# Kernel tuning notes

Measured on AMD Instinct MI355X. Metric: run time of the kernel, lower is better.

The kernel has to match this reference:

```python
import jax, jax.numpy as jnp
import numpy as np

N_HEADS = 16
EMBED_DIM = 1024
HEAD_DIM = EMBED_DIM // N_HEADS
B, S = 4, 2048


def setup_inputs() -> dict:
    key = jax.random.key(0)
    k1, k2, k3, k4 = jax.random.split(key, 4)
    scale = 1.0 / np.sqrt(EMBED_DIM)
    x = jax.random.normal(k1, (B, S, EMBED_DIM), dtype=jnp.float32)
    Wq = jax.random.normal(k2, (EMBED_DIM, EMBED_DIM), dtype=jnp.float32) * scale
    Wk = jax.random.normal(k3, (EMBED_DIM, EMBED_DIM), dtype=jnp.float32) * scale
    Wv = jax.random.normal(k4, (EMBED_DIM, EMBED_DIM), dtype=jnp.float32) * scale
    return {"x": x, "Wq": Wq, "Wk": Wk, "Wv": Wv}


def reference(x, Wq, Wk, Wv):
    b, s, d = x.shape
    # torch nn.Linear(bias=False): y = x @ W.T
    def proj(W):
        return (x @ W.T).reshape(b, s, N_HEADS, HEAD_DIM).transpose(0, 2, 1, 3)  # [b,h,s,hd]
    q, k, v = proj(Wq), proj(Wk), proj(Wv)
    # scores scaled by sqrt(embed_dim) as in the source (not head_dim)
    scores = jnp.einsum('bhqd,bhkd->bhqk', q, k) / jnp.sqrt(jnp.float32(d))
    attn = jax.nn.softmax(scores, axis=-1)
    out = jnp.einsum('bhqk,bhkd->bhqd', attn, v)  # [b,h,s,hd]
    return out.transpose(0, 2, 1, 3).reshape(b, s, d)
```

## Files before the change

### kernel.cpp

```cpp
#include <hip/hip_runtime.h>

#define S_LEN  2048
#define NHEAD  16
#define HDIM   64
#define DMODEL 1024
#define XN     (4 * 2048 * 1024)
#define WN     (1024 * 1024)

typedef float  floatx4 __attribute__((ext_vector_type(4)));
typedef __bf16 bf16x8  __attribute__((ext_vector_type(8)));
typedef __bf16 bf16x4  __attribute__((ext_vector_type(4)));
typedef unsigned int u32;

union B8 {
  bf16x8 v8;
  bf16x4 v4[2];
  __bf16 e[8];
  uint4  u;
};

typedef __attribute__((address_space(1))) u32 gu32;
typedef __attribute__((address_space(3))) u32 lu32;
__device__ __forceinline__ void gld16(const void* g, void* l) {
  __builtin_amdgcn_global_load_lds((const gu32*)g, (lu32*)l, 16, 0, 0);
}

__global__ __launch_bounds__(256) void cvt_kernel(
    const float* __restrict__ x,  const float* __restrict__ Wq,
    const float* __restrict__ Wk, const float* __restrict__ Wv,
    __bf16* __restrict__ xb, __bf16* __restrict__ Wb)
{
  const size_t base = ((size_t)blockIdx.x * 256 + threadIdx.x) * 8;
  const float* src;
  __bf16* dst;
  float scl = 1.0f;
  if (base < XN) {
    src = x + base;
    dst = xb + base;
  } else {
    const size_t j = base - XN;
    const int mat = (int)(j >> 20);
    const size_t o = j & (WN - 1);
    src = (mat == 0 ? Wq : mat == 1 ? Wk : Wv) + o;
    dst = Wb + ((size_t)mat << 20) + o;
    if (mat == 0) scl = 0.045084220027780106f;
  }
  float4 a = *(const float4*)src;
  float4 b = *(const float4*)(src + 4);
  B8 r;
  r.e[0] = (__bf16)(a.x * scl); r.e[1] = (__bf16)(a.y * scl);
  r.e[2] = (__bf16)(a.z * scl); r.e[3] = (__bf16)(a.w * scl);
  r.e[4] = (__bf16)(b.x * scl); r.e[5] = (__bf16)(b.y * scl);
  r.e[6] = (__bf16)(b.z * scl); r.e[7] = (__bf16)(b.w * scl);
  *(bf16x8*)dst = r.v8;
}

__global__ __launch_bounds__(256) void proj_kernel(
    const __bf16* __restrict__ xb, const __bf16* __restrict__ Wb,
    __bf16* __restrict__ Qo, __bf16* __restrict__ Ko, __bf16* __restrict__ Vt)
{
  __shared__ __attribute__((aligned(16))) union {
    struct { __bf16 As[128 * 32]; __bf16 Bs[128 * 32]; } st;
    __bf16 Es[4][64][72];
  } sh;

  const int tid  = threadIdx.x;
  const int lane = tid & 63;
  const int wv   = tid >> 6;
  const int l15  = lane & 15;
  const int quad = lane >> 4;

  const int row0 = blockIdx.y * 128;
  const int n0   = blockIdx.x * 128;
  const int wrow = (wv >> 1) * 64;
  const int wcol = (wv & 1) * 64;

  floatx4 acc[4][4];
  #pragma unroll
  for (int i = 0; i < 4; i++)
    #pragma unroll
    for (int j = 0; j < 4; j++) acc[i][j] = (floatx4)0.0f;

  const int swz = quad ^ ((l15 >> 1) & 3);

  for (int kk = 0; kk < DMODEL; kk += 32) {
    #pragma unroll
    for (int i = 0; i < 2; i++) {
      const int c    = tid + i * 256;
      const int r    = c >> 2;
      const int glog = (c & 3) ^ ((c >> 3) & 3);
      const size_t lofs = (size_t)(wv * 64 + i * 256) * 8;
      gld16(xb + (size_t)(row0 + r) * DMODEL + kk + glog * 8, sh.st.As + lofs);
      gld16(Wb + (size_t)(n0 + r) * DMODEL + kk + glog * 8, sh.st.Bs + lofs);
    }
    __syncthreads();

    B8 af[4], bg[4];
    #pragma unroll
    for (int mb = 0; mb < 4; mb++)
      af[mb].u = *(const uint4*)(sh.st.As + (size_t)(wrow + mb * 16 + l15) * 32 + swz * 8);
    #pragma unroll
    for (int nb = 0; nb < 4; nb++)
      bg[nb].u = *(const uint4*)(sh.st.Bs + (size_t)(wcol + nb * 16 + l15) * 32 + swz * 8);

    #pragma unroll
    for (int mb = 0; mb < 4; mb++)
      #pragma unroll
      for (int nb = 0; nb < 4; nb++)
        acc[mb][nb] = __builtin_amdgcn_mfma_f32_16x16x32_bf16(
            af[mb].v8, bg[nb].v8, acc[mb][nb], 0, 0, 0);
    __syncthreads();
  }

  const int mat   = n0 >> 10;
  const int bb    = (row0 + wrow) >> 11;
  const int sbase = (row0 + wrow) & 2047;
  const int hh    = ((n0 & 1023) + wcol) >> 6;
  __syncthreads();

  if (mat < 2) {
    #pragma unroll
    for (int mb = 0; mb < 4; mb++)
      #pragma unroll
      for (int rr = 0; rr < 4; rr++)
        #pragma unroll
        for (int nb = 0; nb < 4; nb++)
          sh.Es[wv][mb * 16 + quad * 4 + rr][nb * 16 + l15] =
              (__bf16)acc[mb][nb][rr];
    __bf16* Out = (mat == 0) ? Qo : Ko;
    const size_t obase = ((size_t)(bb * NHEAD + hh) * S_LEN + sbase) * HDIM;
    #pragma unroll
    for (int t = 0; t < 8; t++) {
      const int lin = t * 64 + lane;
      const int s = lin >> 3, g = lin & 7;
      *(uint4*)&Out[obase + (size_t)s * HDIM + g * 8] =
          *(const uint4*)&sh.Es[wv][s][g * 8];
    }
  } else {
    #pragma unroll
    for (int mb = 0; mb < 4; mb++)
      #pragma unroll
      for (int nb = 0; nb < 4; nb++) {
        bf16x4 pk = { (__bf16)acc[mb][nb][0], (__bf16)acc[mb][nb][1],
                      (__bf16)acc[mb][nb][2], (__bf16)acc[mb][nb][3] };
        const int col = 32 * (mb >> 1) + 16 * (quad >> 1) + 8 * (quad & 1) +
                        4 * (mb & 1);
        *(bf16x4*)&sh.Es[wv][nb * 16 + l15][col] = pk;
      }
    const size_t vbase = (size_t)(bb * NHEAD + hh) * HDIM * S_LEN;
    #pragma unroll
    for (int t = 0; t < 8; t++) {
      const int lin = t * 64 + lane;
      const int d = lin >> 3, g = lin & 7;
      *(uint4*)&Vt[vbase + (size_t)d * S_LEN + sbase + g * 8] =
          *(const uint4*)&sh.Es[wv][d][g * 8];
    }
  }
}

__global__ __launch_bounds__(256, 2) void attn_kernel(
    const __bf16* __restrict__ Q, const __bf16* __restrict__ K,
    const __bf16* __restrict__ Vt, float* __restrict__ out)
{
  __shared__ __attribute__((aligned(16))) __bf16 Ks[64 * 64];
  __shared__ __attribute__((aligned(16))) __bf16 Vs[64 * 64];

  const int tid  = threadIdx.x;
  const int lane = tid & 63;
  const int wv   = tid >> 6;
  const int l15  = lane & 15;
  const int quad = lane >> 4;

  const int bh = blockIdx.x;
  const int q0 = blockIdx.y * 256;
  const int b  = bh >> 4;
  const int h  = bh & 15;

  const __bf16* Qb = Q  + (size_t)bh * S_LEN * HDIM;
  const __bf16* Kb = K  + (size_t)bh * S_LEN * HDIM;
  const __bf16* Vb = Vt + (size_t)bh * HDIM * S_LEN;

  B8 aq[4][2];
  #pragma unroll
  for (int nb = 0; nb < 4; nb++)
    #pragma unroll
    for (int kc = 0; kc < 2; kc++)
      aq[nb][kc].u = *(const uint4*)
          &Qb[(size_t)(q0 + wv * 64 + nb * 16 + l15) * HDIM + kc * 32 + quad * 8];

  floatx4 o[4][4];
  float rs[4];
  #pragma unroll
  for (int mt = 0; mt < 4; mt++)
    #pragma unroll
    for (int nb = 0; nb < 4; nb++) o[mt][nb] = (floatx4)0.0f;
  #pragma unroll
  for (int nb = 0; nb < 4; nb++) rs[nb] = 0.0f;

  const int swz0 = quad ^ (l15 & 7);
  const int swz1 = (4 + quad) ^ (l15 & 7);

  for (int kv0 = 0; kv0 < S_LEN; kv0 += 64) {
    #pragma unroll
    for (int i = 0; i < 2; i++) {
      const int c    = tid + i * 256;
      const int r    = c >> 3;
      const int glog = (c & 7) ^ ((c >> 3) & 7);
      const size_t lofs = (size_t)(wv * 64 + i * 256) * 8;
      gld16(Kb + (size_t)(kv0 + r) * HDIM + glog * 8, Ks + lofs);
      gld16(Vb + (size_t)r * S_LEN + kv0 + glog * 8, Vs + lofs);
    }
    __syncthreads();

    floatx4 sa[4][4];
    #pragma unroll
    for (int t = 0; t < 4; t++)
      #pragma unroll
      for (int nb = 0; nb < 4; nb++) sa[t][nb] = (floatx4)0.0f;

    #pragma unroll
    for (int kc = 0; kc < 2; kc++) {
      const int sw = kc ? swz1 : swz0;
      B8 ak[4];
      #pragma unroll
      for (int t = 0; t < 4; t++)
        ak[t].u = *(const uint4*)(Ks + (size_t)(t * 16 + l15) * 64 + sw * 8);
      #pragma unroll
      for (int t = 0; t < 4; t++)
        #pragma unroll
        for (int nb = 0; nb < 4; nb++)
          sa[t][nb] = __builtin_amdgcn_mfma_f32_16x16x32_bf16(
              ak[t].v8, aq[nb][kc].v8, sa[t][nb], 0, 0, 0);
    }

    #pragma unroll
    for (int kc = 0; kc < 2; kc++) {
      const int sw = kc ? swz1 : swz0;
      B8 pf[4];
      #pragma unroll
      for (int nb = 0; nb < 4; nb++) {
        float e0 = __builtin_amdgcn_exp2f(sa[2 * kc][nb][0]);
        float e1 = __builtin_amdgcn_exp2f(sa[2 * kc][nb][1]);
        float e2 = __builtin_amdgcn_exp2f(sa[2 * kc][nb][2]);
        float e3 = __builtin_amdgcn_exp2f(sa[2 * kc][nb][3]);
        float e4 = __builtin_amdgcn_exp2f(sa[2 * kc + 1][nb][0]);
        float e5 = __builtin_amdgcn_exp2f(sa[2 * kc + 1][nb][1]);
        float e6 = __builtin_amdgcn_exp2f(sa[2 * kc + 1][nb][2]);
        float e7 = __builtin_amdgcn_exp2f(sa[2 * kc + 1][nb][3]);
        rs[nb] += ((e0 + e1) + (e2 + e3)) + ((e4 + e5) + (e6 + e7));
        pf[nb].e[0] = (__bf16)e0; pf[nb].e[1] = (__bf16)e1;
        pf[nb].e[2] = (__bf16)e2; pf[nb].e[3] = (__bf16)e3;
        pf[nb].e[4] = (__bf16)e4; pf[nb].e[5] = (__bf16)e5;
        pf[nb].e[6] = (__bf16)e6; pf[nb].e[7] = (__bf16)e7;
      }
      B8 av[4];
      #pragma unroll
      for (int mt = 0; mt < 4; mt++)
        av[mt].u = *(const uint4*)(Vs + (size_t)(mt * 16 + l15) * 64 + sw * 8);
      #pragma unroll
      for (int mt = 0; mt < 4; mt++)
        #pragma unroll
        for (int nb = 0; nb < 4; nb++)
          o[mt][nb] = __builtin_amdgcn_mfma_f32_16x16x32_bf16(
              av[mt].v8, pf[nb].v8, o[mt][nb], 0, 0, 0);
    }
    __syncthreads();
  }

  #pragma unroll
  for (int nb = 0; nb < 4; nb++) {
    float v = rs[nb];
    v += __shfl_xor(v, 16);
    v += __shfl_xor(v, 32);
    const float inv = 1.0f / v;
    const int q = q0 + wv * 64 + nb * 16 + l15;
    #pragma unroll
    for (int mt = 0; mt < 4; mt++) {
      float4 w = { o[mt][nb][0] * inv, o[mt][nb][1] * inv,
                   o[mt][nb][2] * inv, o[mt][nb][3] * inv };
      *(float4*)&out[((size_t)(b * S_LEN + q)) * DMODEL + h * HDIM +
                     mt * 16 + quad * 4] = w;
    }
  }
}

extern "C" void kernel_launch(void* const* d_in, const int* in_sizes, int n_in,
                              void* d_out, int out_size, void* d_ws, size_t ws_size,
                              hipStream_t stream) {
  const float* x  = (const float*)d_in[0];
  const float* Wq = (const float*)d_in[1];
  const float* Wk = (const float*)d_in[2];
  const float* Wv = (const float*)d_in[3];
  float* out = (float*)d_out;

  __bf16* xb = (__bf16*)d_ws;
  __bf16* Wb = xb + XN;
  __bf16* Q  = Wb + 3 * (size_t)WN;
  __bf16* K  = Q + (size_t)XN;
  __bf16* Vt = K + (size_t)XN;

  dim3 b256(256);
  cvt_kernel<<<dim3((XN + 3 * WN) / (256 * 8)), b256, 0, stream>>>(
      x, Wq, Wk, Wv, xb, Wb);

  dim3 g1(24, 64);
  proj_kernel<<<g1, b256, 0, stream>>>(xb, Wb, Q, K, Vt);

  dim3 g2(64, 8);
  attn_kernel<<<g2, b256, 0, stream>>>(Q, K, Vt, out);
}
```

Baseline: 218.2 us.

## Double-buffer LDS tiles in projection and attention kernels

Both the projection GEMM and the attention kernel now keep two LDS buffers. The global-to-LDS loads for the next K-tile or KV-tile are issued right after the barrier, so they run while the MFMAs work on the current buffer. This also drops one of the two __syncthreads per iteration. The cost is double the LDS staging footprint, which could reduce occupancy. The overlap also depends on the compiler not inserting a conservative vmcnt wait before the LDS reads.

```diff
diff --git a/kernel.cpp b/kernel.cpp
--- a/kernel.cpp
+++ b/kernel.cpp
@@ -60,7 +60,7 @@
     __bf16* __restrict__ Qo, __bf16* __restrict__ Ko, __bf16* __restrict__ Vt)
 {
   __shared__ __attribute__((aligned(16))) union {
-    struct { __bf16 As[128 * 32]; __bf16 Bs[128 * 32]; } st;
+    struct { __bf16 As[2][128 * 32]; __bf16 Bs[2][128 * 32]; } st;
     __bf16 Es[4][64][72];
   } sh;
 
@@ -83,25 +83,41 @@
 
   const int swz = quad ^ ((l15 >> 1) & 3);
 
+  const int c0    = tid;
+  const int r0_   = c0 >> 2;
+  const int g0    = (c0 & 3) ^ ((c0 >> 3) & 3);
+  const int c1    = tid + 256;
+  const int r1_   = c1 >> 2;
+  const int g1    = (c1 & 3) ^ ((c1 >> 3) & 3);
+  const size_t l0 = (size_t)(wv * 64) * 8;
+  const size_t l1 = (size_t)(wv * 64 + 256) * 8;
+
+  {
+    gld16(xb + (size_t)(row0 + r0_) * DMODEL + 0 + g0 * 8, sh.st.As[0] + l0);
+    gld16(Wb + (size_t)(n0 + r0_) * DMODEL + 0 + g0 * 8, sh.st.Bs[0] + l0);
+    gld16(xb + (size_t)(row0 + r1_) * DMODEL + 0 + g1 * 8, sh.st.As[0] + l1);
+    gld16(Wb + (size_t)(n0 + r1_) * DMODEL + 0 + g1 * 8, sh.st.Bs[0] + l1);
+  }
+
+  int buf = 0;
   for (int kk = 0; kk < DMODEL; kk += 32) {
-    #pragma unroll
-    for (int i = 0; i < 2; i++) {
-      const int c    = tid + i * 256;
-      const int r    = c >> 2;
-      const int glog = (c & 3) ^ ((c >> 3) & 3);
-      const size_t lofs = (size_t)(wv * 64 + i * 256) * 8;
-      gld16(xb + (size_t)(row0 + r) * DMODEL + kk + glog * 8, sh.st.As + lofs);
-      gld16(Wb + (size_t)(n0 + r) * DMODEL + kk + glog * 8, sh.st.Bs + lofs);
-    }
     __syncthreads();
+    if (kk + 32 < DMODEL) {
+      const int nb_ = buf ^ 1;
+      const int k2  = kk + 32;
+      gld16(xb + (size_t)(row0 + r0_) * DMODEL + k2 + g0 * 8, sh.st.As[nb_] + l0);
+      gld16(Wb + (size_t)(n0 + r0_) * DMODEL + k2 + g0 * 8, sh.st.Bs[nb_] + l0);
+      gld16(xb + (size_t)(row0 + r1_) * DMODEL + k2 + g1 * 8, sh.st.As[nb_] + l1);
+      gld16(Wb + (size_t)(n0 + r1_) * DMODEL + k2 + g1 * 8, sh.st.Bs[nb_] + l1);
+    }
 
     B8 af[4], bg[4];
     #pragma unroll
     for (int mb = 0; mb < 4; mb++)
-      af[mb].u = *(const uint4*)(sh.st.As + (size_t)(wrow + mb * 16 + l15) * 32 + swz * 8);
+      af[mb].u = *(const uint4*)(sh.st.As[buf] + (size_t)(wrow + mb * 16 + l15) * 32 + swz * 8);
     #pragma unroll
     for (int nb = 0; nb < 4; nb++)
-      bg[nb].u = *(const uint4*)(sh.st.Bs + (size_t)(wcol + nb * 16 + l15) * 32 + swz * 8);
+      bg[nb].u = *(const uint4*)(sh.st.Bs[buf] + (size_t)(wcol + nb * 16 + l15) * 32 + swz * 8);
 
     #pragma unroll
     for (int mb = 0; mb < 4; mb++)
@@ -109,7 +125,7 @@
       for (int nb = 0; nb < 4; nb++)
         acc[mb][nb] = __builtin_amdgcn_mfma_f32_16x16x32_bf16(
             af[mb].v8, bg[nb].v8, acc[mb][nb], 0, 0, 0);
-    __syncthreads();
+    buf ^= 1;
   }
 
   const int mat   = n0 >> 10;
@@ -162,8 +178,8 @@
     const __bf16* __restrict__ Q, const __bf16* __restrict__ K,
     const __bf16* __restrict__ Vt, float* __restrict__ out)
 {
-  __shared__ __attribute__((aligned(16))) __bf16 Ks[64 * 64];
-  __shared__ __attribute__((aligned(16))) __bf16 Vs[64 * 64];
+  __shared__ __attribute__((aligned(16))) __bf16 Ks[2][64 * 64];
+  __shared__ __attribute__((aligned(16))) __bf16 Vs[2][64 * 64];
 
   const int tid  = threadIdx.x;
   const int lane = tid & 63;
@@ -200,17 +216,31 @@
   const int swz0 = quad ^ (l15 & 7);
   const int swz1 = (4 + quad) ^ (l15 & 7);
 
+  const int rA  = tid >> 3;
+  const int gA  = (tid & 7) ^ ((tid >> 3) & 7);
+  const int rB  = (tid + 256) >> 3;
+  const int gB  = ((tid + 256) & 7) ^ (((tid + 256) >> 3) & 7);
+  const size_t lA = (size_t)(wv * 64) * 8;
+  const size_t lB = (size_t)(wv * 64 + 256) * 8;
+
+  {
+    gld16(Kb + (size_t)rA * HDIM + gA * 8, Ks[0] + lA);
+    gld16(Vb + (size_t)rA * S_LEN + gA * 8, Vs[0] + lA);
+    gld16(Kb + (size_t)rB * HDIM + gB * 8, Ks[0] + lB);
+    gld16(Vb + (size_t)rB * S_LEN + gB * 8, Vs[0] + lB);
+  }
+
+  int buf = 0;
   for (int kv0 = 0; kv0 < S_LEN; kv0 += 64) {
-    #pragma unroll
-    for (int i = 0; i < 2; i++) {
-      const int c    = tid + i * 256;
-      const int r    = c >> 3;
-      const int glog = (c & 7) ^ ((c >> 3) & 7);
-      const size_t lofs = (size_t)(wv * 64 + i * 256) * 8;
-      gld16(Kb + (size_t)(kv0 + r) * HDIM + glog * 8, Ks + lofs);
-      gld16(Vb + (size_t)r * S_LEN + kv0 + glog * 8, Vs + lofs);
-    }
     __syncthreads();
+    if (kv0 + 64 < S_LEN) {
+      const int nbuf = buf ^ 1;
+      const int kv1  = kv0 + 64;
+      gld16(Kb + (size_t)(kv1 + rA) * HDIM + gA * 8, Ks[nbuf] + lA);
+      gld16(Vb + (size_t)rA * S_LEN + kv1 + gA * 8, Vs[nbuf] + lA);
+      gld16(Kb + (size_t)(kv1 + rB) * HDIM + gB * 8, Ks[nbuf] + lB);
+      gld16(Vb + (size_t)rB * S_LEN + kv1 + gB * 8, Vs[nbuf] + lB);
+    }
 
     floatx4 sa[4][4];
     #pragma unroll
@@ -224,7 +254,7 @@
       B8 ak[4];
       #pragma unroll
       for (int t = 0; t < 4; t++)
-        ak[t].u = *(const uint4*)(Ks + (size_t)(t * 16 + l15) * 64 + sw * 8);
+        ak[t].u = *(const uint4*)(Ks[buf] + (size_t)(t * 16 + l15) * 64 + sw * 8);
       #pragma unroll
       for (int t = 0; t < 4; t++)
         #pragma unroll
@@ -256,7 +286,7 @@
       B8 av[4];
       #pragma unroll
       for (int mt = 0; mt < 4; mt++)
-        av[mt].u = *(const uint4*)(Vs + (size_t)(mt * 16 + l15) * 64 + sw * 8);
+        av[mt].u = *(const uint4*)(Vs[buf] + (size_t)(mt * 16 + l15) * 64 + sw * 8);
       #pragma unroll
       for (int mt = 0; mt < 4; mt++)
         #pragma unroll
@@ -264,7 +294,7 @@
           o[mt][nb] = __builtin_amdgcn_mfma_f32_16x16x32_bf16(
               av[mt].v8, pf[nb].v8, o[mt][nb], 0, 0, 0);
     }
-    __syncthreads();
+    buf ^= 1;
   }
 
   #pragma unroll
```

New measurement: 222.9 us. +2.1%, slower.
